# Kernel optimization log

Hardware: AMD Instinct MI355X
Metric: run time of the kernel (lower is better)

## Reference

```python
import jax, jax.numpy as jnp
import numpy as np

BACKBONE_C = 480
NUM_SEG = 4
HIDDEN = 128
IN_DIM = 2 + BACKBONE_C + NUM_SEG + 2  # 488
N_NODES = 200000
N_EDGES = 800000
FH = FW = 128


def _bilinear_sample(feat, vertices, image_size):
    # feat: (C, H, W); vertices: (N, 2) in pixel space.
    # Matches F.grid_sample(..., mode='bilinear', align_corners=True) with
    # grid = vertices/image_size*2 - 1  =>  ix = vx/image_size*(W-1).
    C, H, W = feat.shape
    ix = vertices[:, 0] / image_size * (W - 1)
    iy = vertices[:, 1] / image_size * (H - 1)
    x0 = jnp.floor(ix)
    y0 = jnp.floor(iy)
    wx = ix - x0
    wy = iy - y0
    x0i = jnp.clip(x0.astype(jnp.int32), 0, W - 1)
    x1i = jnp.clip(x0i + 1, 0, W - 1)
    y0i = jnp.clip(y0.astype(jnp.int32), 0, H - 1)
    y1i = jnp.clip(y0i + 1, 0, H - 1)
    f00 = feat[:, y0i, x0i]  # (C, N)
    f01 = feat[:, y0i, x1i]
    f10 = feat[:, y1i, x0i]
    f11 = feat[:, y1i, x1i]
    out = (f00 * (1 - wx) * (1 - wy) + f01 * wx * (1 - wy)
           + f10 * (1 - wx) * wy + f11 * wx * wy)
    return out.T  # (N, C)


def setup_inputs() -> dict:
    key = jax.random.key(0)
    k = jax.random.split(key, 8)
    vertices = jax.random.uniform(k[0], (N_NODES, 2), jnp.float32) * 512.0
    backbone_features = jax.random.normal(k[1], (1, BACKBONE_C, FH, FW), jnp.float32)
    seg_probs = jax.random.uniform(k[2], (1, NUM_SEG, FH, FW), jnp.float32)
    edge_index = jax.random.randint(k[3], (2, N_EDGES), 0, N_NODES, jnp.int64)
    s1 = 1.0 / np.sqrt(IN_DIM)
    s2 = 1.0 / np.sqrt(HIDDEN)
    W1 = jax.random.uniform(k[4], (HIDDEN, IN_DIM), jnp.float32, -s1, s1)
    b1 = jax.random.uniform(k[5], (HIDDEN,), jnp.float32, -s1, s1)
    W2 = jax.random.uniform(k[6], (HIDDEN, HIDDEN), jnp.float32, -s2, s2)
    b2 = jax.random.uniform(k[7], (HIDDEN,), jnp.float32, -s2, s2)
    return {"vertices": vertices, "backbone_features": backbone_features,
            "seg_probs": seg_probs, "edge_index": edge_index,
            "W1": W1, "b1": b1, "W2": W2, "b2": b2, "image_size": 512}


def reference(vertices, backbone_features, seg_probs, edge_index, W1, b1, W2, b2, image_size):
    N = vertices.shape[0]
    coords_norm = vertices / image_size  # (N, 2)
    backbone_feats = _bilinear_sample(backbone_features[0], vertices, image_size)  # (N, C)
    seg_stats = _bilinear_sample(seg_probs[0], vertices, image_size)  # (N, num_seg)
    # degree via scatter-add over both endpoints
    idx = jnp.concatenate([edge_index[0], edge_index[1]]).astype(jnp.int32)
    degree = jax.ops.segment_sum(jnp.ones(idx.shape[0], jnp.float32), idx, num_segments=N)
    degree_norm = degree / (degree.max() + 1e-6)
    # distance to nearest image boundary, normalized by image_size/2
    dx = jnp.minimum(vertices[:, 0], image_size - vertices[:, 0])
    dy = jnp.minimum(vertices[:, 1], image_size - vertices[:, 1])
    dist_to_boundary = jnp.minimum(dx, dy) / (image_size / 2)
    structural = jnp.stack([degree_norm, dist_to_boundary], axis=1)  # (N, 2)
    node_feats = jnp.concatenate([coords_norm, backbone_feats, seg_stats, structural], axis=1)  # (N, 488)
    h = jax.nn.relu(node_feats @ W1.T + b1)
    h = jax.nn.relu(h @ W2.T + b2)
    return h
```

## Files before the change

### kernel.cpp

```cpp
#include <hip/hip_runtime.h>

typedef _Float16 half_t;
typedef __attribute__((ext_vector_type(2))) _Float16 halfx2;
typedef __attribute__((ext_vector_type(8))) _Float16 halfx8;
typedef __attribute__((ext_vector_type(4))) float floatx4;

#define N_NODES 200000
#define N_EDGES 800000
#define NPOS    16384
#define KIN     484

#define NSLICE  32
#define NRANGE  8
#define RNODES  25000
#define RWORDS  6250
#define CWORDS  50000
#define SCHUNK  12500

#define WS_DEGPK 0
#define WS_DEG   6400000
#define WS_MAXD  7200000
#define WS_W2F   7200064
#define WS_W1H   7232832
#define WS_U     7363904

__global__ __launch_bounds__(256) void k0(const float* __restrict__ W1,
                                          const float* __restrict__ W2,
                                          half_t* __restrict__ w2f,
                                          half_t* __restrict__ w1h) {
  const int tid = threadIdx.x, bid = blockIdx.x;
  if (bid == 0) {
    for (int i = tid; i < 128 * 128; i += 256) {
      int k8   = i & 7;
      int l15  = (i >> 3) & 15;
      int q4   = (i >> 7) & 3;
      int ks32 = (i >> 9) & 1;
      int h    = (i >> 10) & 1;
      int t    = i >> 11;
      int row = t * 16 + l15;
      int col = h * 64 + ks32 * 32 + q4 * 8 + k8;
      w2f[i] = (half_t)W2[row * 128 + col];
    }
  } else {
    int j = bid - 1;
    const float* row = W1 + j * 488 + 2;
    int k1 = tid, k2 = tid + 256;
    w1h[j * 512 + k1] = (half_t)((k1 < KIN) ? row[k1] : 0.f);
    w1h[j * 512 + k2] = (half_t)((k2 < KIN) ? row[k2] : 0.f);
  }
}

__global__ __launch_bounds__(256) void k1(const half_t* __restrict__ w1h,
                                          const float* __restrict__ bb,
                                          const float* __restrict__ seg,
                                          const int* __restrict__ e,
                                          unsigned* __restrict__ degpk,
                                          half_t* __restrict__ U) {
  __shared__ __align__(16) char sm[25600];

  const int tid = threadIdx.x;
  const int bid = blockIdx.x;

  if (bid < 256) {
    half_t* Bl = (half_t*)sm;
    half_t* Ol = (half_t*)(sm + 5120);

    const int n0 = bid * 64;
    const int wave = tid >> 6, lane = tid & 63;
    const int l15 = lane & 15, q8 = (lane >> 4) * 8;

    floatx4 acc[2][4];
    for (int mt = 0; mt < 2; ++mt)
      for (int nt = 0; nt < 4; ++nt)
        acc[mt][nt] = (floatx4){0.f, 0.f, 0.f, 0.f};

    for (int kb = 0; kb < 512; kb += 32) {
      halfx8 af[2];
      for (int mt = 0; mt < 2; ++mt)
        af[mt] = *(const halfx8*)&w1h[(wave * 32 + mt * 16 + l15) * 512 + kb + q8];

      {
        int kk = tid >> 3, nc = (tid & 7) * 8;
        int k = kb + kk;
        float vals[8];
        if (k < 480) {
          const float* src = bb + k * NPOS + n0 + nc;
          float4 a = *(const float4*)(src);
          float4 b = *(const float4*)(src + 4);
          vals[0] = a.x; vals[1] = a.y; vals[2] = a.z; vals[3] = a.w;
          vals[4] = b.x; vals[5] = b.y; vals[6] = b.z; vals[7] = b.w;
        } else if (k < KIN) {
          const float* src = seg + (k - 480) * NPOS + n0 + nc;
          float4 a = *(const float4*)(src);
          float4 b = *(const float4*)(src + 4);
          vals[0] = a.x; vals[1] = a.y; vals[2] = a.z; vals[3] = a.w;
          vals[4] = b.x; vals[5] = b.y; vals[6] = b.z; vals[7] = b.w;
        } else {
          for (int i = 0; i < 8; ++i) vals[i] = 0.f;
        }
        for (int i = 0; i < 8; ++i) Bl[(nc + i) * 40 + kk] = (half_t)vals[i];
      }
      __syncthreads();

      halfx8 bf[4];
      for (int nt = 0; nt < 4; ++nt)
        bf[nt] = *(const halfx8*)&Bl[(nt * 16 + l15) * 40 + q8];
      for (int mt = 0; mt < 2; ++mt)
        for (int nt = 0; nt < 4; ++nt)
          acc[mt][nt] = __builtin_amdgcn_mfma_f32_16x16x32_f16(af[mt], bf[nt],
                                                               acc[mt][nt], 0, 0, 0);
      __syncthreads();
    }

    for (int mt = 0; mt < 2; ++mt)
      for (int nt = 0; nt < 4; ++nt)
        for (int r = 0; r < 4; ++r) {
          int j = wave * 32 + mt * 16 + (lane >> 4) * 4 + r;
          int n = nt * 16 + l15;
          Ol[n * 136 + j] = (half_t)acc[mt][nt][r];
        }
    __syncthreads();
    for (int it = 0; it < 4; ++it) {
      int idx = tid + it * 256;
      int n = idx >> 4, c8 = (idx & 15) * 8;
      *(halfx8*)(U + (long)(n0 + n) * 128 + c8) = *(const halfx8*)&Ol[n * 136 + c8];
    }
  } else {
    unsigned* cnt = (unsigned*)sm;
    const int hb = bid - 256;
    const int s  = hb >> 3;
    const int r  = hb & 7;
    const int lo = r * RNODES;
    const int lane = tid & 63;

    for (int i = tid; i < 64 + RWORDS; i += 256) cnt[i] = 0;
    __syncthreads();

#define HBIN(v) { unsigned d = (unsigned)(v) - (unsigned)lo;                 \
                  bool ok = d < (unsigned)RNODES;                            \
                  unsigned w = ok ? (d >> 2) + 64u : (unsigned)lane;         \
                  unsigned a_ = ok ? (1u << ((d & 3u) << 3)) : 0u;           \
                  atomicAdd(&cnt[w], a_); }

    const int4* E4 = (const int4*)e + s * SCHUNK;
    for (int base = 0; base < 12288; base += 1024) {
      int4 a = E4[base + tid];
      int4 b = E4[base + tid + 256];
      int4 c = E4[base + tid + 512];
      int4 d4 = E4[base + tid + 768];
      HBIN(a.x); HBIN(a.y); HBIN(a.z); HBIN(a.w);
      HBIN(b.x); HBIN(b.y); HBIN(b.z); HBIN(b.w);
      HBIN(c.x); HBIN(c.y); HBIN(c.z); HBIN(c.w);
      HBIN(d4.x); HBIN(d4.y); HBIN(d4.z); HBIN(d4.w);
    }
    if (tid < SCHUNK - 12288) {
      int4 a = E4[12288 + tid];
      HBIN(a.x); HBIN(a.y); HBIN(a.z); HBIN(a.w);
    }
#undef HBIN
    __syncthreads();

    unsigned* dst = degpk + s * CWORDS + r * RWORDS;
    for (int i = tid; i < RWORDS; i += 256) dst[i] = cnt[64 + i];
  }
}

__global__ __launch_bounds__(256) void k2(const unsigned* __restrict__ degpk,
                                          unsigned* __restrict__ deg,
                                          unsigned* __restrict__ maxd) {
  const int w4 = blockIdx.x * 256 + threadIdx.x;
  unsigned m = 0;
  if (w4 < CWORDS / 4) {
    uint4 s = make_uint4(0u, 0u, 0u, 0u);
    for (int c = 0; c < NSLICE; ++c) {
      uint4 v = *(const uint4*)&degpk[c * CWORDS + w4 * 4];
      s.x += v.x; s.y += v.y; s.z += v.z; s.w += v.w;
    }
    unsigned words[4] = {s.x, s.y, s.z, s.w};
    for (int k = 0; k < 4; ++k) {
      unsigned sw = words[k];
      uint4 o = make_uint4(sw & 255u, (sw >> 8) & 255u,
                           (sw >> 16) & 255u, sw >> 24);
      *(uint4*)&deg[w4 * 16 + k * 4] = o;
      m = max(m, max(max(o.x, o.y), max(o.z, o.w)));
    }
  }
  for (int off = 32; off > 0; off >>= 1) {
    unsigned o = (unsigned)__shfl_down((int)m, off);
    m = max(m, o);
  }
  if ((threadIdx.x & 63) == 0) atomicMax(maxd, m);
}

__global__ __launch_bounds__(256, 8) void k_main(const float* __restrict__ vertices,
                                              const float* __restrict__ W1,
                                              const float* __restrict__ b1,
                                              const float* __restrict__ b2,
                                              const unsigned* __restrict__ deg,
                                              const unsigned* __restrict__ maxd,
                                              const half_t* __restrict__ U,
                                              const half_t* __restrict__ w2f,
                                              float* __restrict__ out) {
  __shared__ half_t At[64 * 136];
  __shared__ int   pPos[64];
  __shared__ float pW[4][64];
  __shared__ float pE[4][64];
  __shared__ float b2l[128];

  const int tid = threadIdx.x;
  const int nodeBase = blockIdx.x * 64;

  if (tid < 128) b2l[tid] = b2[tid];

  if (tid < 64) {
    int n = nodeBase + tid;
    float vx = vertices[2 * n], vy = vertices[2 * n + 1];
    float ix = vx * (127.0f / 512.0f), iy = vy * (127.0f / 512.0f);
    float fx = floorf(ix), fy = floorf(iy);
    float wx = ix - fx, wy = iy - fy;
    int x0 = min(max((int)fx, 0), 127);
    int y0 = min(max((int)fy, 0), 127);
    pPos[tid] = y0 * 128 + x0;
    pW[0][tid] = (1.f - wx) * (1.f - wy);
    pW[1][tid] = wx * (1.f - wy);
    pW[2][tid] = (1.f - wx) * wy;
    pW[3][tid] = wx * wy;
    pE[0][tid] = vx * (1.f / 512.f);
    pE[1][tid] = vy * (1.f / 512.f);
    float md = (float)(*maxd) + 1e-6f;
    pE[2][tid] = (float)deg[n] / md;
    float dx = fminf(vx, 512.f - vx), dy = fminf(vy, 512.f - vy);
    pE[3][tid] = fminf(dx, dy) * (1.f / 256.f);
  }

  const int jp = tid & 63, q = tid >> 6;
  const int j2 = jp * 2;
  const float* r0 = W1 + j2 * 488;
  const float* r1 = r0 + 488;
  float c00 = r0[0], c01 = r0[1], c06 = r0[486], c07 = r0[487];
  float c10 = r1[0], c11 = r1[1], c16 = r1[486], c17 = r1[487];
  float bb0 = b1[j2], bb1 = b1[j2 + 1];
  __syncthreads();

#pragma unroll 4
  for (int it = 0; it < 16; ++it) {
    int ln = it * 4 + q;
    int pos = pPos[ln];
    float w00 = pW[0][ln], w01 = pW[1][ln], w10 = pW[2][ln], w11 = pW[3][ln];
    float cx = pE[0][ln], cy = pE[1][ln], dn = pE[2][ln], db = pE[3][ln];
    const half_t* base = U + (long)pos * 128 + j2;
    halfx2 u00 = *(const halfx2*)(base);
    halfx2 u01 = *(const halfx2*)(base + 128);
    halfx2 u10 = *(const halfx2*)(base + 16384);
    halfx2 u11 = *(const halfx2*)(base + 16512);
    float z0 = bb0 + c00 * cx + c01 * cy + c06 * dn + c07 * db
             + w00 * (float)u00.x + w01 * (float)u01.x
             + w10 * (float)u10.x + w11 * (float)u11.x;
    float z1 = bb1 + c10 * cx + c11 * cy + c16 * dn + c17 * db
             + w00 * (float)u00.y + w01 * (float)u01.y
             + w10 * (float)u10.y + w11 * (float)u11.y;
    halfx2 h;
    h.x = (half_t)fmaxf(z0, 0.f);
    h.y = (half_t)fmaxf(z1, 0.f);
    *(halfx2*)&At[ln * 136 + j2] = h;
  }
  __syncthreads();

  const int wave = tid >> 6, lane = tid & 63;
  const int l15 = lane & 15, q4 = lane >> 4;
  const half_t* wf = w2f + (q4 * 16 + l15) * 8;
  floatx4 acc[8];
  for (int t = 0; t < 8; ++t) acc[t] = (floatx4){0.f, 0.f, 0.f, 0.f};

  for (int h = 0; h < 2; ++h)
    for (int ks32 = 0; ks32 < 2; ++ks32) {
      halfx8 af = *(const halfx8*)&At[(wave * 16 + l15) * 136 + h * 64 +
                                      ks32 * 32 + q4 * 8];
      for (int t = 0; t < 8; ++t) {
        halfx8 bf = *(const halfx8*)&wf[(t * 4 + h * 2 + ks32) * 512];
        acc[t] = __builtin_amdgcn_mfma_f32_16x16x32_f16(af, bf, acc[t], 0, 0, 0);
      }
    }

  for (int t = 0; t < 8; ++t) {
    int col = t * 16 + l15;
    float bias = b2l[col];
    int row0 = nodeBase + wave * 16 + q4 * 4;
    for (int r = 0; r < 4; ++r)
      out[(long)(row0 + r) * 128 + col] = fmaxf(acc[t][r] + bias, 0.f);
  }
}

extern "C" void kernel_launch(void* const* d_in, const int* in_sizes, int n_in,
                              void* d_out, int out_size, void* d_ws, size_t ws_size,
                              hipStream_t stream) {
  const float* vertices = (const float*)d_in[0];
  const float* bb       = (const float*)d_in[1];
  const float* seg      = (const float*)d_in[2];
  const int*   edges    = (const int*)d_in[3];
  const float* W1       = (const float*)d_in[4];
  const float* b1       = (const float*)d_in[5];
  const float* W2       = (const float*)d_in[6];
  const float* b2       = (const float*)d_in[7];

  char* ws = (char*)d_ws;
  unsigned* degpk = (unsigned*)(ws + WS_DEGPK);
  unsigned* deg   = (unsigned*)(ws + WS_DEG);
  unsigned* maxd  = (unsigned*)(ws + WS_MAXD);
  half_t*   w2f   = (half_t*)(ws + WS_W2F);
  half_t*   w1h   = (half_t*)(ws + WS_W1H);
  half_t*   U     = (half_t*)(ws + WS_U);
  float*    outp  = (float*)d_out;

  hipMemsetAsync(ws + WS_MAXD, 0, 64, stream);
  k0<<<129, 256, 0, stream>>>(W1, W2, w2f, w1h);
  k1<<<256 + NSLICE * NRANGE, 256, 0, stream>>>(w1h, bb, seg, edges, degpk, U);
  k2<<<49, 256, 0, stream>>>(degpk, deg, maxd);
  k_main<<<3125, 256, 0, stream>>>(vertices, W1, b1, b2, deg, maxd, U, w2f, outp);
}
```

Baseline: 214.2 us.

## Pre-transpose backbone features to fp16 and restructure per-pixel W1 GEMM

Adds a pass that transposes and converts the backbone and segmentation maps into an fp16 pixel-major buffer. It merges the weight preparation, the maxd reset and the degree histogram into one launch, which drops the separate k0 kernel and the memset. The W1 GEMM kernel then reads pre-swizzled MFMA fragments directly from global memory, with no shared-memory staging or barriers in the K loop. The cost is an extra 16 MB round trip through global memory for the transposed buffer, and the transpose itself reads with narrow scalar loads.

```diff
diff --git a/kernel.cpp b/kernel.cpp
--- a/kernel.cpp
+++ b/kernel.cpp
@@ -17,121 +17,55 @@
 #define CWORDS  50000
 #define SCHUNK  12500
 
+#define KT_TRANS 4096
+#define KT_HISTO (KT_TRANS + NSLICE * NRANGE)
+#define KT_W1F   (KT_HISTO + 8)
+#define KT_GRID  (KT_W1F + 1)
+
 #define WS_DEGPK 0
 #define WS_DEG   6400000
 #define WS_MAXD  7200000
 #define WS_W2F   7200064
-#define WS_W1H   7232832
+#define WS_W1F   7232832
 #define WS_U     7363904
-
-__global__ __launch_bounds__(256) void k0(const float* __restrict__ W1,
-                                          const float* __restrict__ W2,
-                                          half_t* __restrict__ w2f,
-                                          half_t* __restrict__ w1h) {
-  const int tid = threadIdx.x, bid = blockIdx.x;
-  if (bid == 0) {
-    for (int i = tid; i < 128 * 128; i += 256) {
-      int k8   = i & 7;
-      int l15  = (i >> 3) & 15;
-      int q4   = (i >> 7) & 3;
-      int ks32 = (i >> 9) & 1;
-      int h    = (i >> 10) & 1;
-      int t    = i >> 11;
-      int row = t * 16 + l15;
-      int col = h * 64 + ks32 * 32 + q4 * 8 + k8;
-      w2f[i] = (half_t)W2[row * 128 + col];
-    }
-  } else {
-    int j = bid - 1;
-    const float* row = W1 + j * 488 + 2;
-    int k1 = tid, k2 = tid + 256;
-    w1h[j * 512 + k1] = (half_t)((k1 < KIN) ? row[k1] : 0.f);
-    w1h[j * 512 + k2] = (half_t)((k2 < KIN) ? row[k2] : 0.f);
-  }
-}
-
-__global__ __launch_bounds__(256) void k1(const half_t* __restrict__ w1h,
-                                          const float* __restrict__ bb,
+#define WS_BT    11558208
+
+__global__ __launch_bounds__(256) void kT(const float* __restrict__ bb,
                                           const float* __restrict__ seg,
                                           const int* __restrict__ e,
+                                          const float* __restrict__ W1,
+                                          const float* __restrict__ W2,
                                           unsigned* __restrict__ degpk,
-                                          half_t* __restrict__ U) {
+                                          half_t* __restrict__ Bt,
+                                          half_t* __restrict__ w1f,
+                                          half_t* __restrict__ w2f,
+                                          unsigned* __restrict__ maxd) {
   __shared__ __align__(16) char sm[25600];
 
   const int tid = threadIdx.x;
   const int bid = blockIdx.x;
-
-  if (bid < 256) {
-    half_t* Bl = (half_t*)sm;
-    half_t* Ol = (half_t*)(sm + 5120);
-
-    const int n0 = bid * 64;
-    const int wave = tid >> 6, lane = tid & 63;
-    const int l15 = lane & 15, q8 = (lane >> 4) * 8;
-
-    floatx4 acc[2][4];
-    for (int mt = 0; mt < 2; ++mt)
-      for (int nt = 0; nt < 4; ++nt)
-        acc[mt][nt] = (floatx4){0.f, 0.f, 0.f, 0.f};
-
-    for (int kb = 0; kb < 512; kb += 32) {
-      halfx8 af[2];
-      for (int mt = 0; mt < 2; ++mt)
-        af[mt] = *(const halfx8*)&w1h[(wave * 32 + mt * 16 + l15) * 512 + kb + q8];
-
-      {
-        int kk = tid >> 3, nc = (tid & 7) * 8;
-        int k = kb + kk;
-        float vals[8];
-        if (k < 480) {
-          const float* src = bb + k * NPOS + n0 + nc;
-          float4 a = *(const float4*)(src);
-          float4 b = *(const float4*)(src + 4);
-          vals[0] = a.x; vals[1] = a.y; vals[2] = a.z; vals[3] = a.w;
-          vals[4] = b.x; vals[5] = b.y; vals[6] = b.z; vals[7] = b.w;
-        } else if (k < KIN) {
-          const float* src = seg + (k - 480) * NPOS + n0 + nc;
-          float4 a = *(const float4*)(src);
-          float4 b = *(const float4*)(src + 4);
-          vals[0] = a.x; vals[1] = a.y; vals[2] = a.z; vals[3] = a.w;
-          vals[4] = b.x; vals[5] = b.y; vals[6] = b.z; vals[7] = b.w;
-        } else {
-          for (int i = 0; i < 8; ++i) vals[i] = 0.f;
-        }
-        for (int i = 0; i < 8; ++i) Bl[(nc + i) * 40 + kk] = (half_t)vals[i];
-      }
-      __syncthreads();
-
-      halfx8 bf[4];
-      for (int nt = 0; nt < 4; ++nt)
-        bf[nt] = *(const halfx8*)&Bl[(nt * 16 + l15) * 40 + q8];
-      for (int mt = 0; mt < 2; ++mt)
-        for (int nt = 0; nt < 4; ++nt)
-          acc[mt][nt] = __builtin_amdgcn_mfma_f32_16x16x32_f16(af[mt], bf[nt],
-                                                               acc[mt][nt], 0, 0, 0);
-      __syncthreads();
-    }
-
-    for (int mt = 0; mt < 2; ++mt)
-      for (int nt = 0; nt < 4; ++nt)
-        for (int r = 0; r < 4; ++r) {
-          int j = wave * 32 + mt * 16 + (lane >> 4) * 4 + r;
-          int n = nt * 16 + l15;
-          Ol[n * 136 + j] = (half_t)acc[mt][nt][r];
-        }
-    __syncthreads();
-    for (int it = 0; it < 4; ++it) {
-      int idx = tid + it * 256;
-      int n = idx >> 4, c8 = (idx & 15) * 8;
-      *(halfx8*)(U + (long)(n0 + n) * 128 + c8) = *(const halfx8*)&Ol[n * 136 + c8];
-    }
-  } else {
+  const int wave = tid >> 6, lane = tid & 63;
+  const int l15 = lane & 15, q4 = lane >> 4;
+
+  if (bid < KT_TRANS) {
+    const int pt = bid >> 4, kt = bid & 15;
+    const int p0 = pt * 64, kb = kt * 32;
+    const int kw = kb + wave * 8;
+    halfx8 h;
+    for (int i = 0; i < 8; ++i) {
+      int k = kw + i;
+      float v = 0.f;
+      if (k < 480)      v = bb[(long)k * NPOS + p0 + lane];
+      else if (k < KIN) v = seg[(long)(k - 480) * NPOS + p0 + lane];
+      h[i] = (half_t)v;
+    }
+    *(halfx8*)&Bt[(long)(p0 + lane) * 512 + kw] = h;
+  } else if (bid < KT_HISTO) {
     unsigned* cnt = (unsigned*)sm;
-    const int hb = bid - 256;
+    const int hb = bid - KT_TRANS;
     const int s  = hb >> 3;
     const int r  = hb & 7;
     const int lo = r * RNODES;
-    const int lane = tid & 63;
 
     for (int i = tid; i < 64 + RWORDS; i += 256) cnt[i] = 0;
     __syncthreads();
@@ -162,6 +96,64 @@
 
     unsigned* dst = degpk + s * CWORDS + r * RWORDS;
     for (int i = tid; i < RWORDS; i += 256) dst[i] = cnt[64 + i];
+  } else if (bid < KT_W1F) {
+    const int t = bid - KT_HISTO;
+    const int j = t * 16 + l15;
+    for (int c = 0; c < 4; ++c) {
+      int kbi = c * 4 + wave;
+      halfx8 h;
+      for (int i = 0; i < 8; ++i) {
+        int k = kbi * 32 + q4 * 8 + i;
+        h[i] = (half_t)((k < KIN) ? W1[j * 488 + 2 + k] : 0.f);
+      }
+      *(halfx8*)&w1f[(t * 16 + kbi) * 512 + lane * 8] = h;
+    }
+  } else {
+    if (tid == 0) *maxd = 0u;
+    for (int i = tid; i < 128 * 128; i += 256) {
+      int k8   = i & 7;
+      int il15 = (i >> 3) & 15;
+      int iq4  = (i >> 7) & 3;
+      int ks32 = (i >> 9) & 1;
+      int hh   = (i >> 10) & 1;
+      int t    = i >> 11;
+      int row = t * 16 + il15;
+      int col = hh * 64 + ks32 * 32 + iq4 * 8 + k8;
+      w2f[i] = (half_t)W2[row * 128 + col];
+    }
+  }
+}
+
+__global__ __launch_bounds__(256) void k1(const half_t* __restrict__ Bt,
+                                          const half_t* __restrict__ w1f,
+                                          half_t* __restrict__ U) {
+  __shared__ half_t Ol[64 * 136];
+
+  const int tid = threadIdx.x, bid = blockIdx.x;
+  const int wave = tid >> 6, lane = tid & 63;
+  const int l15 = lane & 15, q4 = lane >> 4;
+  const int n0 = bid * 64;
+
+  floatx4 acc[8];
+  for (int t = 0; t < 8; ++t) acc[t] = (floatx4){0.f, 0.f, 0.f, 0.f};
+
+  const half_t* bt = Bt + (long)(n0 + wave * 16 + l15) * 512 + q4 * 8;
+  for (int kbi = 0; kbi < 16; ++kbi) {
+    halfx8 af = *(const halfx8*)&bt[kbi * 32];
+    for (int t = 0; t < 8; ++t) {
+      halfx8 bf = *(const halfx8*)&w1f[(t * 16 + kbi) * 512 + lane * 8];
+      acc[t] = __builtin_amdgcn_mfma_f32_16x16x32_f16(af, bf, acc[t], 0, 0, 0);
+    }
+  }
+
+  for (int t = 0; t < 8; ++t)
+    for (int r = 0; r < 4; ++r)
+      Ol[(wave * 16 + q4 * 4 + r) * 136 + t * 16 + l15] = (half_t)acc[t][r];
+  __syncthreads();
+  for (int it = 0; it < 4; ++it) {
+    int idx = tid + it * 256;
+    int n = idx >> 4, c8 = (idx & 15) * 8;
+    *(halfx8*)(U + (long)(n0 + n) * 128 + c8) = *(const halfx8*)&Ol[n * 136 + c8];
   }
 }
 
@@ -308,13 +300,13 @@
   unsigned* deg   = (unsigned*)(ws + WS_DEG);
   unsigned* maxd  = (unsigned*)(ws + WS_MAXD);
   half_t*   w2f   = (half_t*)(ws + WS_W2F);
-  half_t*   w1h   = (half_t*)(ws + WS_W1H);
+  half_t*   w1f   = (half_t*)(ws + WS_W1F);
   half_t*   U     = (half_t*)(ws + WS_U);
+  half_t*   Bt    = (half_t*)(ws + WS_BT);
   float*    outp  = (float*)d_out;
 
-  hipMemsetAsync(ws + WS_MAXD, 0, 64, stream);
-  k0<<<129, 256, 0, stream>>>(W1, W2, w2f, w1h);
-  k1<<<256 + NSLICE * NRANGE, 256, 0, stream>>>(w1h, bb, seg, edges, degpk, U);
+  kT<<<KT_GRID, 256, 0, stream>>>(bb, seg, edges, W1, W2, degpk, Bt, w1f, w2f, maxd);
+  k1<<<256, 256, 0, stream>>>(Bt, w1f, U);
   k2<<<49, 256, 0, stream>>>(degpk, deg, maxd);
   k_main<<<3125, 256, 0, stream>>>(vertices, W1, b1, b2, deg, maxd, U, w2f, outp);
 }
```

New measurement: 222.7 us. 4.0% more time.
